# Performance work log

Hardware: AMD Instinct MI355X
Metric: run time of the kernel (lower is better)

## Reference

```python
import jax, jax.numpy as jnp
import numpy as np

N = 2048        # number of entities
D = 2048        # entity_dimensionality
HEADS = 16
HD = D // HEADS  # per-head dim = 128
ROUNDS = 2
LAYERS = 2


def setup_inputs() -> dict:
    key = jax.random.key(0)
    ks = jax.random.split(key, 12)
    s = 1.0 / np.sqrt(D)  # keep activations O(1)
    inp = {
        "entities": jax.random.normal(ks[0], (N, D), jnp.float32),
        "Wq": jax.random.normal(ks[1], (D, D), jnp.float32) * s,
        "bq": jnp.zeros((D,), jnp.float32),
        "Wk": jax.random.normal(ks[2], (D, D), jnp.float32) * s,
        "bk": jnp.zeros((D,), jnp.float32),
        "Wv": jax.random.normal(ks[3], (D, D), jnp.float32) * s,
        "bv": jnp.zeros((D,), jnp.float32),
        "W0": jax.random.normal(ks[4], (D, D), jnp.float32) * s,
        "b0": jnp.zeros((D,), jnp.float32),
        "W1": jax.random.normal(ks[5], (D, D), jnp.float32) * s,
        "b1": jnp.zeros((D,), jnp.float32),
    }
    return inp


def _linear(x, W, b):
    # torch nn.Linear: y = x @ W.T + b
    return x @ W.T + b


def _split_heads(x):
    # [N, D] -> [H, N, hd]
    return x.reshape(N, HEADS, HD).transpose(1, 0, 2)


def reference(entities, Wq, bq, Wk, bk, Wv, bv, W0, b0, W1, b1):
    scale = 1.0 / np.sqrt(HD)
    for _ in range(ROUNDS):
        q = _split_heads(_linear(entities, Wq, bq))  # [H, N, hd]
        k = _split_heads(_linear(entities, Wk, bk))
        v = _split_heads(_linear(entities, Wv, bv))
        scores = jnp.einsum('hqd,hkd->hqk', q, k) * scale  # [H, N, N]
        attn = jax.nn.softmax(scores, axis=-1)
        o = jnp.einsum('hqk,hkd->hqd', attn, v)            # [H, N, hd]
        o = o.transpose(1, 0, 2).reshape(N, D)             # merge heads
        o = jax.nn.relu(_linear(o, W0, b0))
        o = jax.nn.relu(_linear(o, W1, b1))
        entities = entities + o  # residual=True
    return entities
```

## Files before the change

### kernel.cpp

```cpp
#include <hip/hip_runtime.h>
#include <stdint.h>

#define DIM   2048
#define NENT  2048
#define NHEAD 16
#define HD    128

typedef unsigned short u16;
typedef u16   u16x4  __attribute__((ext_vector_type(4)));
typedef u16   u16x8  __attribute__((ext_vector_type(8)));
typedef float f32x4  __attribute__((ext_vector_type(4)));
typedef float f32x16 __attribute__((ext_vector_type(16)));
typedef __bf16 bf16x8 __attribute__((ext_vector_type(8)));

#define MFMA16(a, b, c) __builtin_amdgcn_mfma_f32_16x16x32_bf16((a), (b), (c), 0, 0, 0)
#define MFMA32(a, b, c) __builtin_amdgcn_mfma_f32_32x32x16_bf16((a), (b), (c), 0, 0, 0)

#define SMUL 0.12751743f

__device__ __forceinline__ u16 f2b(float f) {
  union { float f; unsigned int u; } x; x.f = f;
  unsigned int r = x.u + 0x7FFFu + ((x.u >> 16) & 1u);
  return (u16)(r >> 16);
}
__device__ __forceinline__ float b2f(u16 b) {
  union { unsigned int u; float f; } x; x.u = ((unsigned int)b) << 16;
  return x.f;
}
__device__ __forceinline__ unsigned int cvtpk(float a, float b) {
  unsigned int r;
  asm("v_cvt_pk_bf16_f32 %0, %1, %2" : "=v"(r) : "v"(a), "v"(b));
  return r;
}
__device__ __forceinline__ float exp2_fast(float x) {
  float r;
  asm("v_exp_f32 %0, %1" : "=v"(r) : "v"(x));
  return r;
}

__device__ __forceinline__ void async16(const void* g, void* l) {
  __builtin_amdgcn_global_load_lds(
      (const __attribute__((address_space(1))) unsigned int*)(uintptr_t)g,
      (__attribute__((address_space(3))) unsigned int*)(uintptr_t)l, 16, 0, 0);
}

__global__ void __launch_bounds__(256) conv6_k(
    const float* __restrict__ s0, const float* __restrict__ s1,
    const float* __restrict__ s2, const float* __restrict__ s3,
    const float* __restrict__ s4, const float* __restrict__ s5,
    u16* __restrict__ d0, u16* __restrict__ d1, u16* __restrict__ d2,
    u16* __restrict__ d3, u16* __restrict__ d4, u16* __restrict__ d5) {
  int sel = blockIdx.y;
  const float* s = sel == 0 ? s0 : sel == 1 ? s1 : sel == 2 ? s2
                 : sel == 3 ? s3 : sel == 4 ? s4 : s5;
  u16* d = sel == 0 ? d0 : sel == 1 ? d1 : sel == 2 ? d2
         : sel == 3 ? d3 : sel == 4 ? d4 : d5;
  int i = blockIdx.x * 256 + threadIdx.x;
  float4 v = ((const float4*)s)[i];
  u16x4 o;
  o.x = f2b(v.x); o.y = f2b(v.y); o.z = f2b(v.z); o.w = f2b(v.w);
  *(u16x4*)(d + (size_t)i * 4) = o;
}

template <int MODE>
__device__ __forceinline__ void gemm128_body(
    u16* sbuf,
    const u16* __restrict__ A, const u16* __restrict__ Bw,
    const float* __restrict__ bias, u16* __restrict__ C,
    int brow0, int bcol0, int kbase, int NT, float oscale) {
  u16* lA = sbuf;
  u16* lB = sbuf + 8192;
  const int tid = threadIdx.x;
  const int lane = tid & 63, w = tid >> 6;
  const int wr = w >> 1, wc = w & 1;
  const int l15 = lane & 15;
  const int koff = (lane >> 4) * 8;
  const int swz = (l15 & 7) << 3;

  f32x4 acc[4][4];
#pragma unroll
  for (int m = 0; m < 4; m++)
#pragma unroll
    for (int n = 0; n < 4; n++) acc[m][n] = (f32x4)0.f;

  const int lr = w * 8 + (lane >> 3);
  const int scol = ((lane & 7) ^ (lr & 7)) * 8;

#pragma unroll 1
  for (int kt = 0; kt < NT; kt++) {
    const int colg = kbase + kt * 64 + scol;
#pragma unroll
    for (int i = 0; i < 4; i++) {
      async16(A + (size_t)(brow0 + i * 32 + lr) * DIM + colg,
              lA + i * 2048 + w * 512);
      async16(Bw + (size_t)(bcol0 + i * 32 + lr) * DIM + colg,
              lB + i * 2048 + w * 512);
    }
    __syncthreads();
#pragma unroll
    for (int kk = 0; kk < 2; kk++) {
      bf16x8 af[4], bfr[4];
#pragma unroll
      for (int m = 0; m < 4; m++)
        af[m] = *(const bf16x8*)(lA + (wr * 64 + m * 16 + l15) * 64 +
                                 ((kk * 32 + koff) ^ swz));
#pragma unroll
      for (int n = 0; n < 4; n++)
        bfr[n] = *(const bf16x8*)(lB + (wc * 64 + n * 16 + l15) * 64 +
                                  ((kk * 32 + koff) ^ swz));
#pragma unroll
      for (int m = 0; m < 4; m++)
#pragma unroll
        for (int n = 0; n < 4; n++)
          acc[m][n] = MFMA16(af[m], bfr[n], acc[m][n]);
    }
    __syncthreads();
  }

  if (MODE == 2) {
    u16* arena = sbuf + w * 4096;
#pragma unroll
    for (int n = 0; n < 4; n++) {
      int c_loc = n * 16 + l15;
      float bv = bias[bcol0 + wc * 64 + c_loc];
#pragma unroll
      for (int m = 0; m < 4; m++)
#pragma unroll
        for (int r = 0; r < 4; r++) {
          int r_loc = m * 16 + (lane >> 4) * 4 + r;
          arena[c_loc * 64 + (r_loc ^ ((c_loc & 7) * 8))] =
              f2b(acc[m][n][r] + bv);
        }
    }
    __syncthreads();
    const int h = (bcol0 + wc * 64) >> 7;
    const int d0 = (bcol0 + wc * 64) & 127;
    const int R0 = brow0 + wr * 64;
    u16* vbase = C + (size_t)h * HD * NENT + R0;
#pragma unroll
    for (int it = 0; it < 8; it++) {
      int d_loc = it * 8 + (lane >> 3);
      int r0 = (lane & 7) * 8;
      u16x8 val = *(const u16x8*)(arena + d_loc * 64 + (r0 ^ ((d_loc & 7) * 8)));
      *(u16x8*)(vbase + (size_t)(d0 + d_loc) * NENT + r0) = val;
    }
    return;
  }

#pragma unroll
  for (int n = 0; n < 4; n++) {
    int col = bcol0 + wc * 64 + n * 16 + l15;
    float bv = (MODE == 0) ? bias[col] : 0.f;
#pragma unroll
    for (int m = 0; m < 4; m++) {
#pragma unroll
      for (int r = 0; r < 4; r++) {
        int row = brow0 + wr * 64 + m * 16 + (lane >> 4) * 4 + r;
        float val = acc[m][n][r] + bv;
        if (MODE == 0) val *= oscale;
        C[(size_t)row * DIM + col] = f2b(val);
      }
    }
  }
}

__global__ void __launch_bounds__(256, 3) gemm128_qkv_k(
    const u16* __restrict__ A,
    const u16* __restrict__ Bq, const u16* __restrict__ Bk, const u16* __restrict__ Bv,
    const float* __restrict__ bq, const float* __restrict__ bk, const float* __restrict__ bv,
    u16* __restrict__ q, u16* __restrict__ k, u16* __restrict__ vt) {
  __shared__ u16 sbuf[2 * 128 * 64];
  int x = blockIdx.x & 7;
  int j = blockIdx.x >> 3;
  int bn48 = x * 6 + j % 6;
  int bm = j / 6;
  int sel = bn48 >> 4, bnn = bn48 & 15;
  if (sel == 2) {
    gemm128_body<2>(sbuf, A, Bv, bv, vt, bm * 128, bnn * 128, 0, 32, 1.f);
  } else {
    const u16* B = sel == 0 ? Bq : Bk;
    const float* bias = sel == 0 ? bq : bk;
    u16* Cc = sel == 0 ? q : k;
    gemm128_body<0>(sbuf, A, B, bias, Cc, bm * 128, bnn * 128, 0, 32,
                    sel == 0 ? SMUL : 1.f);
  }
}

__global__ void __launch_bounds__(256, 3) gemm128_sk3_k(
    const u16* __restrict__ A, const u16* __restrict__ Bw,
    u16* __restrict__ p0, u16* __restrict__ p1, u16* __restrict__ p2) {
  __shared__ u16 sbuf[2 * 128 * 64];
  int x = blockIdx.x & 7;
  int j = blockIdx.x >> 3;
  int rem = j % 6;
  int bn = 2 * x + (rem & 1);
  int sk = rem >> 1;
  int bm = j / 6;
  u16* part = sk == 0 ? p0 : (sk == 1 ? p1 : p2);
  int nt = (sk == 2) ? 10 : 11;
  gemm128_body<1>(sbuf, A, Bw, nullptr, part, bm * 128, bn * 128,
                  sk * 11 * 64, nt, 1.f);
}

template <int RESID, int WB>
__global__ void __launch_bounds__(256) reduce3_k(
    const u16* __restrict__ p0, const u16* __restrict__ p1,
    const u16* __restrict__ p2,
    const float* __restrict__ bias, const float* __restrict__ resid,
    float* __restrict__ outf, u16* __restrict__ outb) {
  int i = blockIdx.x * 256 + threadIdx.x;
  u16x8 a0 = ((const u16x8*)p0)[i];
  u16x8 a1 = ((const u16x8*)p1)[i];
  u16x8 a2 = ((const u16x8*)p2)[i];
  size_t base = (size_t)i * 8;
  int col = (int)(base & (DIM - 1));
  u16x8 ob;
  float of[8];
#pragma unroll
  for (int j = 0; j < 8; j++) {
    float s = b2f(a0[j]) + b2f(a1[j]) + b2f(a2[j]) + bias[col + j];
    s = fmaxf(s, 0.f);
    if (RESID) {
      float o = resid[base + j] + s;
      of[j] = o;
      if (WB) ob[j] = f2b(o);
    } else {
      ob[j] = f2b(s);
    }
  }
  if (WB) *(u16x8*)(outb + base) = ob;
  if (RESID) {
#pragma unroll
    for (int j = 0; j < 8; j++) outf[base + j] = of[j];
  }
}

__global__ void __launch_bounds__(256, 2) attn_k(
    const u16* __restrict__ q, const u16* __restrict__ kmat,
    const u16* __restrict__ vt, u16* __restrict__ oz0, u16* __restrict__ oz1,
    float* __restrict__ ml) {
  const int h = blockIdx.x, qb = blockIdx.y, kvs = blockIdx.z;
  u16* __restrict__ oz = kvs ? oz1 : oz0;
  __shared__ u16 lK[2][64 * 128];
  __shared__ u16 lV[2][128 * 64];
  const int tid = threadIdx.x, lane = tid & 63, w = tid >> 6;
  const int l31 = lane & 31, hl = lane >> 5;
  const int r4 = lane >> 4, r8 = lane >> 3;
  const int c16e = (lane & 15) * 8, c8e = (lane & 7) * 8;
  const int swz = (l31 & 7) << 3;
  const u16* vhead = vt + (size_t)h * HD * NENT;
  const int kv0 = kvs * (NENT / 2);

  const int qrow = qb * 128 + w * 32 + l31;
  const u16* qptr = q + (size_t)qrow * DIM + h * HD + hl * 8;
  bf16x8 qf[8];
#pragma unroll
  for (int ks = 0; ks < 8; ks++)
    qf[ks] = *(const bf16x8*)(qptr + ks * 16);

  auto stageKV = [&](int kt, int buf) {
    const size_t krow0 = (size_t)kv0 + kt * 64;
#pragma unroll
    for (int c = 0; c < 4; c++) {
      int ch = w * 4 + c;
      int krow = ch * 4 + r4;
      async16(kmat + (krow0 + krow) * DIM + h * HD + (c16e ^ ((krow & 7) << 3)),
              lK[buf] + ch * 512);
      int vrow = ch * 8 + r8;
      async16(vhead + (size_t)vrow * NENT + krow0 + (c8e ^ ((r8 & 7) << 3)),
              lV[buf] + ch * 512);
    }
  };

  f32x16 Oacc[4];
#pragma unroll
  for (int dt = 0; dt < 4; dt++) Oacc[dt] = (f32x16)0.f;
  float m_i = -1e30f, l_i = 0.f;

  stageKV(0, 0);
  int cur = 0;

#pragma unroll 1
  for (int kt = 0; kt < NENT / 2 / 64; kt++) {
    __syncthreads();
    if (kt + 1 < NENT / 2 / 64) stageKV(kt + 1, cur ^ 1);
    const u16* Kc = lK[cur];
    const u16* Vc = lV[cur];

    f32x16 sA = (f32x16)0.f, sB = (f32x16)0.f;
#pragma unroll
    for (int ks = 0; ks < 8; ks++) {
      bf16x8 a0 = *(const bf16x8*)(Kc + l31 * 128 + ((ks * 16 + hl * 8) ^ swz));
      sA = MFMA32(a0, qf[ks], sA);
      bf16x8 a1 = *(const bf16x8*)(Kc + (32 + l31) * 128 + ((ks * 16 + hl * 8) ^ swz));
      sB = MFMA32(a1, qf[ks], sB);
    }

    float pmax = sA[0];
#pragma unroll
    for (int i = 1; i < 16; i++) pmax = fmaxf(pmax, sA[i]);
#pragma unroll
    for (int i = 0; i < 16; i++) pmax = fmaxf(pmax, sB[i]);
    pmax = fmaxf(pmax, __shfl_xor(pmax, 32));
    bool resc = __any(pmax > m_i + 8.f);
    float corr = 1.f;
    if (resc) {
      float mn = fmaxf(m_i, pmax);
      corr = exp2_fast(m_i - mn);
      m_i = mn;
    }
    float ls = 0.f;
#pragma unroll
    for (int i = 0; i < 16; i++) { sA[i] = exp2_fast(sA[i] - m_i); ls += sA[i]; }
#pragma unroll
    for (int i = 0; i < 16; i++) { sB[i] = exp2_fast(sB[i] - m_i); ls += sB[i]; }
    l_i = l_i * corr + ls;
    if (resc) {
#pragma unroll
      for (int r = 0; r < 16; r++) {
        int qo = hl * 4 + (r & 3) + 8 * (r >> 2);
        float cr = __shfl(corr, qo);
        Oacc[0][r] *= cr; Oacc[1][r] *= cr; Oacc[2][r] *= cr; Oacc[3][r] *= cr;
      }
    }

#pragma unroll
    for (int ks = 0; ks < 4; ks++) {
      const f32x16& p = (ks < 2) ? sA : sB;
      const int E = ((2 * ks) & 3) * 4;
      const int Od = ((2 * ks + 1) & 3) * 4;
      unsigned int e0 = cvtpk(p[E + 0], p[E + 1]);
      unsigned int e1 = cvtpk(p[E + 2], p[E + 3]);
      unsigned int o0 = cvtpk(p[Od + 0], p[Od + 1]);
      unsigned int o1 = cvtpk(p[Od + 2], p[Od + 3]);
      asm volatile("v_permlane32_swap_b32 %0, %1" : "+v"(e0), "+v"(o0));
      asm volatile("v_permlane32_swap_b32 %0, %1" : "+v"(e1), "+v"(o1));
      union { unsigned int u[4]; bf16x8 v; } pk;
      pk.u[0] = e0; pk.u[1] = e1; pk.u[2] = o0; pk.u[3] = o1;
#pragma unroll
      for (int dt = 0; dt < 4; dt++) {
        bf16x8 b = *(const bf16x8*)(Vc + (dt * 32 + l31) * 64 +
                                    ((ks * 16 + hl * 8) ^ swz));
        Oacc[dt] = MFMA32(pk.v, b, Oacc[dt]);
      }
    }
    cur ^= 1;
  }

  float lt = l_i + __shfl_xor(l_i, 32);
  if (hl == 0) {
    float* mlp = ml + ((size_t)(kvs * NHEAD + h) * NENT + qrow) * 2;
    mlp[0] = m_i;
    mlp[1] = lt;
  }
#pragma unroll
  for (int r = 0; r < 16; r++) {
    int row = qb * 128 + w * 32 + hl * 4 + (r & 3) + 8 * (r >> 2);
#pragma unroll
    for (int dt = 0; dt < 4; dt++)
      oz[(size_t)row * DIM + h * HD + dt * 32 + l31] = f2b(Oacc[dt][r]);
  }
}

__global__ void __launch_bounds__(256) combine_k(
    const u16* __restrict__ O0, const u16* __restrict__ O1,
    const float* __restrict__ ml, u16* __restrict__ o) {
  int i = blockIdx.x * 256 + threadIdx.x;
  size_t base = (size_t)i * 8;
  int row = (int)(base >> 11);
  int h = ((int)base & (DIM - 1)) >> 7;
  const float* p0 = ml + ((size_t)h * NENT + row) * 2;
  const float* p1 = ml + ((size_t)(NHEAD + h) * NENT + row) * 2;
  float m0 = p0[0], l0 = p0[1];
  float m1 = p1[0], l1 = p1[1];
  float M = fmaxf(m0, m1);
  float w0 = exp2_fast(m0 - M), w1 = exp2_fast(m1 - M);
  float inv = 1.f / (l0 * w0 + l1 * w1);
  w0 *= inv; w1 *= inv;
  u16x8 a = ((const u16x8*)O0)[i], b = ((const u16x8*)O1)[i];
  u16x8 r;
#pragma unroll
  for (int j = 0; j < 8; j++) r[j] = f2b(b2f(a[j]) * w0 + b2f(b[j]) * w1);
  ((u16x8*)o)[i] = r;
}

extern "C" void kernel_launch(void* const* d_in, const int* in_sizes, int n_in,
                              void* d_out, int out_size, void* d_ws, size_t ws_size,
                              hipStream_t stream) {
  const float* ent_in = (const float*)d_in[0];
  const float* Wq = (const float*)d_in[1];
  const float* bq = (const float*)d_in[2];
  const float* Wk = (const float*)d_in[3];
  const float* bk = (const float*)d_in[4];
  const float* Wv = (const float*)d_in[5];
  const float* bv = (const float*)d_in[6];
  const float* W0 = (const float*)d_in[7];
  const float* b0 = (const float*)d_in[8];
  const float* W1 = (const float*)d_in[9];
  const float* b1 = (const float*)d_in[10];
  float* out = (float*)d_out;

  char* ws = (char*)d_ws;
  const size_t SZ = (size_t)DIM * DIM * 2;
  u16* wqb = (u16*)ws; ws += SZ;
  u16* wkb = (u16*)ws; ws += SZ;
  u16* wvb = (u16*)ws; ws += SZ;
  u16* w0b = (u16*)ws; ws += SZ;
  u16* w1b = (u16*)ws; ws += SZ;
  u16* entb = (u16*)ws; ws += SZ;
  u16* qb_ = (u16*)ws; ws += SZ;
  u16* kb_ = (u16*)ws; ws += SZ;
  u16* vb_ = (u16*)ws; ws += SZ;
  u16* vtb = (u16*)ws; ws += SZ;
  u16* ob_ = (u16*)ws; ws += SZ;
  u16* h1b = (u16*)ws; ws += SZ;

  conv6_k<<<dim3(4096, 6), 256, 0, stream>>>(Wq, Wk, Wv, W0, W1, ent_in,
                                             wqb, wkb, wvb, w0b, w1b, entb);

  for (int r = 0; r < 2; r++) {
    const float* cur = r ? (const float*)out : ent_in;
    gemm128_qkv_k<<<768, 256, 0, stream>>>(entb, wqb, wkb, wvb, bq, bk, bv,
                                           qb_, kb_, vtb);
    attn_k<<<dim3(16, 16, 2), 256, 0, stream>>>(qb_, kb_, vtb, vb_, h1b,
                                                (float*)entb);
    combine_k<<<2048, 256, 0, stream>>>(vb_, h1b, (const float*)entb, ob_);
    gemm128_sk3_k<<<768, 256, 0, stream>>>(ob_, w0b, entb, qb_, kb_);
    reduce3_k<0, 1><<<2048, 256, 0, stream>>>(entb, qb_, kb_, b0, nullptr,
                                              nullptr, h1b);
    gemm128_sk3_k<<<768, 256, 0, stream>>>(h1b, w1b, entb, qb_, kb_);
    if (r == 0)
      reduce3_k<1, 1><<<2048, 256, 0, stream>>>(entb, qb_, kb_, b1, cur,
                                                out, entb);
    else
      reduce3_k<1, 0><<<2048, 256, 0, stream>>>(entb, qb_, kb_, b1, cur,
                                                out, entb);
  }
}
```

Before: 355.5 us.

## Replace 128x128 split-K-3 MLP GEMM with 256x256 split-K-4 kernel

The two MLP projection GEMMs move from 128x128 tiles with a 3-way K split (768 blocks of 256 threads) to 256x256 tiles with a 4-way K split (256 blocks of 512 threads). The new body double-buffers LDS tiles loaded asynchronously and interleaves barriers with setprio around the MFMA bursts. Larger tiles raise arithmetic intensity and cut global reloads of A and B. In exchange the kernel uses more LDS and registers per block, and the reduce kernel now reads and sums four bf16 partial buffers instead of three.

```diff
diff --git a/kernel.cpp b/kernel.cpp
--- a/kernel.cpp
+++ b/kernel.cpp
@@ -186,39 +186,135 @@
   }
 }
 
-__global__ void __launch_bounds__(256, 3) gemm128_sk3_k(
+__device__ __forceinline__ void gemm256sk_body(
     const u16* __restrict__ A, const u16* __restrict__ Bw,
-    u16* __restrict__ p0, u16* __restrict__ p1, u16* __restrict__ p2) {
-  __shared__ u16 sbuf[2 * 128 * 64];
+    u16* __restrict__ C, int brow0, int bcol0, int kbase, int NT) {
+  __shared__ u16 lds[2][4][128 * 64];
+  const int tid = threadIdx.x;
+  const int lane = tid & 63, w = tid >> 6;
+  const int wr = w >> 2, wc = w & 3;
+  const int l15 = lane & 15;
+  const int koff = (lane >> 4) * 8;
+  const int swz = (l15 & 7) << 3;
+
+  f32x4 acc[8][4];
+#pragma unroll
+  for (int m = 0; m < 8; m++)
+#pragma unroll
+    for (int n = 0; n < 4; n++) acc[m][n] = (f32x4)0.f;
+
+  const int srow = lane >> 3;
+  const int scol = ((lane & 7) ^ srow) * 8;
+
+  auto stageTile = [&](int kt) {
+    const int slot = kt & 1;
+    const int colg = kbase + kt * 64 + scol;
+    const u16* Ab = A + (size_t)(brow0 + w * 16 + srow) * DIM + colg;
+    const u16* Bb = Bw + (size_t)(bcol0 + w * 16 + srow) * DIM + colg;
+    u16* d0 = &lds[slot][0][w * 1024];
+    u16* d1 = &lds[slot][1][w * 1024];
+    u16* d2 = &lds[slot][2][w * 1024];
+    u16* d3 = &lds[slot][3][w * 1024];
+    async16(Ab, d0);
+    async16(Ab + 8 * DIM, d0 + 512);
+    async16(Ab + 128 * DIM, d1);
+    async16(Ab + 136 * DIM, d1 + 512);
+    async16(Bb, d2);
+    async16(Bb + 8 * DIM, d2 + 512);
+    async16(Bb + 128 * DIM, d3);
+    async16(Bb + 136 * DIM, d3 + 512);
+  };
+
+  stageTile(0);
+
+#pragma unroll 1
+  for (int kt = 0; kt < NT; kt++) {
+    const int slot = kt & 1;
+    const u16* Ah = &lds[slot][wr][0];
+    const u16* Bh = &lds[slot][2 + (wc >> 1)][0];
+    const int brw = (wc & 1) * 64;
+
+    if (kt + 1 < NT) {
+      stageTile(kt + 1);
+      asm volatile("s_waitcnt vmcnt(8)" ::: "memory");
+    } else {
+      asm volatile("s_waitcnt vmcnt(0)" ::: "memory");
+    }
+    __builtin_amdgcn_s_barrier();
+
+    bf16x8 bfr[4];
+#pragma unroll
+    for (int kk = 0; kk < 2; kk++) {
+#pragma unroll
+      for (int mh = 0; mh < 2; mh++) {
+        if (mh == 0) {
+#pragma unroll
+          for (int n = 0; n < 4; n++)
+            bfr[n] = *(const bf16x8*)(Bh + (brw + n * 16 + l15) * 64 +
+                                      ((kk * 32 + koff) ^ swz));
+        }
+        bf16x8 af[4];
+#pragma unroll
+        for (int m = 0; m < 4; m++)
+          af[m] = *(const bf16x8*)(Ah + (mh * 64 + m * 16 + l15) * 64 +
+                                   ((kk * 32 + koff) ^ swz));
+        __builtin_amdgcn_s_barrier();
+        __builtin_amdgcn_s_setprio(1);
+#pragma unroll
+        for (int m = 0; m < 4; m++)
+#pragma unroll
+          for (int n = 0; n < 4; n++)
+            acc[mh * 4 + m][n] = MFMA16(af[m], bfr[n], acc[mh * 4 + m][n]);
+        __builtin_amdgcn_s_setprio(0);
+        __builtin_amdgcn_s_barrier();
+      }
+    }
+  }
+
+#pragma unroll
+  for (int n = 0; n < 4; n++) {
+    int col = bcol0 + wc * 64 + n * 16 + l15;
+#pragma unroll
+    for (int m = 0; m < 8; m++) {
+#pragma unroll
+      for (int r = 0; r < 4; r++) {
+        int row = brow0 + wr * 128 + m * 16 + (lane >> 4) * 4 + r;
+        C[(size_t)row * DIM + col] = f2b(acc[m][n][r]);
+      }
+    }
+  }
+}
+
+__global__ void __launch_bounds__(512, 2) gemm256_sk4_k(
+    const u16* __restrict__ A, const u16* __restrict__ Bw,
+    u16* __restrict__ p0, u16* __restrict__ p1,
+    u16* __restrict__ p2, u16* __restrict__ p3) {
   int x = blockIdx.x & 7;
   int j = blockIdx.x >> 3;
-  int rem = j % 6;
-  int bn = 2 * x + (rem & 1);
-  int sk = rem >> 1;
-  int bm = j / 6;
-  u16* part = sk == 0 ? p0 : (sk == 1 ? p1 : p2);
-  int nt = (sk == 2) ? 10 : 11;
-  gemm128_body<1>(sbuf, A, Bw, nullptr, part, bm * 128, bn * 128,
-                  sk * 11 * 64, nt, 1.f);
+  int sk = j & 3;
+  int bm = j >> 2;
+  u16* part = sk == 0 ? p0 : (sk == 1 ? p1 : (sk == 2 ? p2 : p3));
+  gemm256sk_body(A, Bw, part, bm * 256, x * 256, sk * 512, 8);
 }
 
 template <int RESID, int WB>
-__global__ void __launch_bounds__(256) reduce3_k(
+__global__ void __launch_bounds__(256) reduce4_k(
     const u16* __restrict__ p0, const u16* __restrict__ p1,
-    const u16* __restrict__ p2,
+    const u16* __restrict__ p2, const u16* __restrict__ p3,
     const float* __restrict__ bias, const float* __restrict__ resid,
     float* __restrict__ outf, u16* __restrict__ outb) {
   int i = blockIdx.x * 256 + threadIdx.x;
   u16x8 a0 = ((const u16x8*)p0)[i];
   u16x8 a1 = ((const u16x8*)p1)[i];
   u16x8 a2 = ((const u16x8*)p2)[i];
+  u16x8 a3 = ((const u16x8*)p3)[i];
   size_t base = (size_t)i * 8;
   int col = (int)(base & (DIM - 1));
   u16x8 ob;
   float of[8];
 #pragma unroll
   for (int j = 0; j < 8; j++) {
-    float s = b2f(a0[j]) + b2f(a1[j]) + b2f(a2[j]) + bias[col + j];
+    float s = b2f(a0[j]) + b2f(a1[j]) + b2f(a2[j]) + b2f(a3[j]) + bias[col + j];
     s = fmaxf(s, 0.f);
     if (RESID) {
       float o = resid[base + j] + s;
@@ -425,15 +521,15 @@
     attn_k<<<dim3(16, 16, 2), 256, 0, stream>>>(qb_, kb_, vtb, vb_, h1b,
                                                 (float*)entb);
     combine_k<<<2048, 256, 0, stream>>>(vb_, h1b, (const float*)entb, ob_);
-    gemm128_sk3_k<<<768, 256, 0, stream>>>(ob_, w0b, entb, qb_, kb_);
-    reduce3_k<0, 1><<<2048, 256, 0, stream>>>(entb, qb_, kb_, b0, nullptr,
-                                              nullptr, h1b);
-    gemm128_sk3_k<<<768, 256, 0, stream>>>(h1b, w1b, entb, qb_, kb_);
+    gemm256_sk4_k<<<256, 512, 0, stream>>>(ob_, w0b, entb, qb_, kb_, vb_);
+    reduce4_k<0, 1><<<2048, 256, 0, stream>>>(entb, qb_, kb_, vb_, b0,
+                                              nullptr, nullptr, h1b);
+    gemm256_sk4_k<<<256, 512, 0, stream>>>(h1b, w1b, entb, qb_, kb_, vb_);
     if (r == 0)
-      reduce3_k<1, 1><<<2048, 256, 0, stream>>>(entb, qb_, kb_, b1, cur,
+      reduce4_k<1, 1><<<2048, 256, 0, stream>>>(entb, qb_, kb_, vb_, b1, cur,
                                                 out, entb);
     else
-      reduce3_k<1, 0><<<2048, 256, 0, stream>>>(entb, qb_, kb_, b1, cur,
+      reduce4_k<1, 0><<<2048, 256, 0, stream>>>(entb, qb_, kb_, vb_, b1, cur,
                                                 out, entb);
   }
 }
```

Result: slower. 391.0 us (+10.0%).
